# Optimization experiments

Hardware: AMD Instinct MI355X
Metric: run time of the kernel (lower is better)

The kernel has to match this reference:

```python
import jax, jax.numpy as jnp
import numpy as np

B, N_CITY, EC, VOCAB = 4096, 50, 128, 40000


def setup_inputs() -> dict:
    key = jax.random.key(0)
    k1, k2, k3, k4 = jax.random.split(key, 4)
    x = jax.random.normal(k1, (B, EC), dtype=jnp.float32)
    top_city_emb = jax.random.normal(k2, (B, N_CITY, EC), dtype=jnp.float32)
    top_city_id = jax.random.randint(k3, (B, N_CITY), 0, VOCAB)
    prob = jnp.zeros((B, VOCAB), dtype=jnp.float32)
    # nn.Linear(EC, EC) params
    W = jax.random.normal(k4, (EC, EC), dtype=jnp.float32) * (1.0 / np.sqrt(EC))
    b = jnp.zeros((EC,), dtype=jnp.float32)
    return {"x": x, "top_city_emb": top_city_emb, "top_city_id": top_city_id,
            "prob": prob, "W": W, "b": b}


def reference(x, top_city_emb, top_city_id, prob, W, b):
    # Linear projection (torch Linear: x @ W^T + b)
    emb_pred = x @ W.T + b                                  # [B, EC]
    # Broadcast dot-product score against candidate embeddings
    scores = jnp.einsum('be,bne->bn', emb_pred, top_city_emb)  # [B, N_CITY]
    p = jax.nn.softmax(scores, axis=1)                      # [B, N_CITY]
    # Scatter-add softmax probs into the vocab-sized output
    rows = jnp.arange(p.shape[0])[:, None]                  # [B, 1] -> broadcast to [B, N_CITY]
    rows = jnp.broadcast_to(rows, top_city_id.shape)
    out = jnp.zeros_like(prob).at[rows, top_city_id].add(p) + 1e-6
    return out
```

## Files before the change

### kernel.cpp

```cpp
#include <hip/hip_runtime.h>
#include <hip/hip_bf16.h>

#define NC    50
#define EC    128
#define VOCAB 40000

__global__ __launch_bounds__(256)
void EmbDotSoftMax_wtpack_kernel(const float* __restrict__ W,
                                 float4*      __restrict__ WTp)
{
    const int idx = blockIdx.x * 256 + threadIdx.x;
    if (idx < (EC / 4) * EC) {
        const int k4 = idx >> 7;
        const int e  = idx & 127;
        WTp[idx] = reinterpret_cast<const float4*>(W)[e * (EC / 4) + k4];
    }
}

__global__ __launch_bounds__(128)
void EmbDotSoftMax_scatter_kernel(const float*  __restrict__ x,
                                  const float*  __restrict__ emb,
                                  const int*    __restrict__ ids,
                                  const float4* __restrict__ WTp,
                                  const float*  __restrict__ bias,
                                  float*        __restrict__ out)
{
    const int b   = blockIdx.x;
    const int tid = threadIdx.x;
    const int w   = tid >> 6;
    const int l   = tid & 63;

    __shared__ float4 x_s4[EC / 4];
    __shared__ float  pred_s[EC];
    __shared__ float  score_s[NC];

    float* out_row = out + (size_t)b * VOCAB;

    if (tid < EC / 4)
        x_s4[tid] = reinterpret_cast<const float4*>(x + (size_t)b * EC)[tid];
    __syncthreads();

    const bool is_score_lane = (l < NC / 2);
    const int  city          = w * (NC / 2) + l;
    const float4* er =
        reinterpret_cast<const float4*>(emb + ((size_t)b * NC + city) * EC);
    float4 pf0, pf1, pf2, pf3, pf4, pf5, pf6, pf7;
    if (is_score_lane) {
        pf0 = er[0]; pf1 = er[1]; pf2 = er[2]; pf3 = er[3];
        pf4 = er[4]; pf5 = er[5]; pf6 = er[6]; pf7 = er[7];
    }

    {
        float acc = 0.0f;
        #pragma unroll
        for (int k4 = 0; k4 < EC / 4; ++k4) {
            const float4 wv = WTp[k4 * EC + tid];
            const float4 xv = x_s4[k4];
            acc = fmaf(wv.x, xv.x, acc);
            acc = fmaf(wv.y, xv.y, acc);
            acc = fmaf(wv.z, xv.z, acc);
            acc = fmaf(wv.w, xv.w, acc);
        }
        pred_s[tid] = acc + bias[tid];
    }
    __syncthreads();

    if (is_score_lane) {
        const float4* p4 = reinterpret_cast<const float4*>(pred_s);
        float acc = 0.0f;
        {
            float4 pv;
            pv = p4[0]; acc = fmaf(pf0.x, pv.x, acc); acc = fmaf(pf0.y, pv.y, acc);
                        acc = fmaf(pf0.z, pv.z, acc); acc = fmaf(pf0.w, pv.w, acc);
            pv = p4[1]; acc = fmaf(pf1.x, pv.x, acc); acc = fmaf(pf1.y, pv.y, acc);
                        acc = fmaf(pf1.z, pv.z, acc); acc = fmaf(pf1.w, pv.w, acc);
            pv = p4[2]; acc = fmaf(pf2.x, pv.x, acc); acc = fmaf(pf2.y, pv.y, acc);
                        acc = fmaf(pf2.z, pv.z, acc); acc = fmaf(pf2.w, pv.w, acc);
            pv = p4[3]; acc = fmaf(pf3.x, pv.x, acc); acc = fmaf(pf3.y, pv.y, acc);
                        acc = fmaf(pf3.z, pv.z, acc); acc = fmaf(pf3.w, pv.w, acc);
            pv = p4[4]; acc = fmaf(pf4.x, pv.x, acc); acc = fmaf(pf4.y, pv.y, acc);
                        acc = fmaf(pf4.z, pv.z, acc); acc = fmaf(pf4.w, pv.w, acc);
            pv = p4[5]; acc = fmaf(pf5.x, pv.x, acc); acc = fmaf(pf5.y, pv.y, acc);
                        acc = fmaf(pf5.z, pv.z, acc); acc = fmaf(pf5.w, pv.w, acc);
            pv = p4[6]; acc = fmaf(pf6.x, pv.x, acc); acc = fmaf(pf6.y, pv.y, acc);
                        acc = fmaf(pf6.z, pv.z, acc); acc = fmaf(pf6.w, pv.w, acc);
            pv = p4[7]; acc = fmaf(pf7.x, pv.x, acc); acc = fmaf(pf7.y, pv.y, acc);
                        acc = fmaf(pf7.z, pv.z, acc); acc = fmaf(pf7.w, pv.w, acc);
        }
        #pragma unroll
        for (int j = 8; j < EC / 4; ++j) {
            const float4 e4 = er[j];
            const float4 pv = p4[j];
            acc = fmaf(e4.x, pv.x, acc);
            acc = fmaf(e4.y, pv.y, acc);
            acc = fmaf(e4.z, pv.z, acc);
            acc = fmaf(e4.w, pv.w, acc);
        }
        score_s[city] = acc;
    }
    __syncthreads();

    if (tid < NC) {
        float m = -1e30f;
        #pragma unroll
        for (int n = 0; n < NC; ++n) m = fmaxf(m, score_s[n]);
        float sum = 0.0f;
        #pragma unroll
        for (int n = 0; n < NC; ++n) sum += __expf(score_s[n] - m);
        const float p  = __expf(score_s[tid] - m) / sum;
        const int   id = ids[(size_t)b * NC + tid];
        atomicAdd(out_row + id, p);
    }
}

__global__ __launch_bounds__(128)
void EmbDotSoftMax_scatter_fb(const float* __restrict__ x,
                              const float* __restrict__ emb,
                              const int*   __restrict__ ids,
                              const float* __restrict__ W,
                              const float* __restrict__ bias,
                              float*       __restrict__ out)
{
    const int b   = blockIdx.x;
    const int tid = threadIdx.x;
    const int w   = tid >> 6;
    const int l   = tid & 63;
    __shared__ float pred_s[EC];
    __shared__ float scores_s[NC];
    float* out_row = out + (size_t)b * VOCAB;
    {
        const float x0 = x[(size_t)b * EC + l];
        const float x1 = x[(size_t)b * EC + 64 + l];
        const float* Wbase = W + (size_t)w * 64 * EC;
        float mine = 0.0f;
        #pragma unroll 8
        for (int i = 0; i < 64; ++i) {
            const float* row = Wbase + i * EC;
            float part = fmaf(x0, row[l], x1 * row[l + 64]);
            #pragma unroll
            for (int off = 32; off; off >>= 1)
                part += __shfl_xor(part, off);
            if (i == l) mine = part;
        }
        pred_s[w * 64 + l] = mine + bias[w * 64 + l];
    }
    __syncthreads();
    {
        const float p0 = pred_s[l];
        const float p1 = pred_s[l + 64];
        const float* base = emb + (size_t)b * NC * EC + (size_t)w * (NC / 2) * EC;
        float part[NC / 2];
        #pragma unroll
        for (int i = 0; i < NC / 2; ++i) {
            const float* er2 = base + i * EC;
            part[i] = fmaf(p0, er2[l], p1 * er2[l + 64]);
        }
        #pragma unroll
        for (int off = 32; off; off >>= 1) {
            #pragma unroll
            for (int i = 0; i < NC / 2; ++i)
                part[i] += __shfl_xor(part[i], off);
        }
        if (l == 0) {
            #pragma unroll
            for (int i = 0; i < NC / 2; ++i)
                scores_s[w * (NC / 2) + i] = part[i];
        }
    }
    __syncthreads();
    if (tid < NC) {
        float m = -1e30f;
        #pragma unroll
        for (int n = 0; n < NC; ++n) m = fmaxf(m, scores_s[n]);
        float sum = 0.0f;
        #pragma unroll
        for (int n = 0; n < NC; ++n) sum += __expf(scores_s[n] - m);
        const float p = __expf(scores_s[tid] - m) / sum;
        atomicAdd(out_row + ids[(size_t)b * NC + tid], p);
    }
}

extern "C" void kernel_launch(void* const* d_in, const int* in_sizes, int n_in,
                              void* d_out, int out_size, void* d_ws, size_t ws_size,
                              hipStream_t stream) {
    const float* x    = (const float*)d_in[0];
    const float* emb  = (const float*)d_in[1];
    const int*   ids  = (const int*)d_in[2];
    const float* W    = (const float*)d_in[4];
    const float* bias = (const float*)d_in[5];
    float*       out  = (float*)d_out;

    const int B = in_sizes[0] / EC;
    const size_t ws_needed = (size_t)(EC / 4) * EC * sizeof(float4);

    hipMemsetAsync(d_out, 0, (size_t)out_size * sizeof(float), stream);

    if (ws_size >= ws_needed) {
        float4* WTp = (float4*)d_ws;
        hipLaunchKernelGGL(EmbDotSoftMax_wtpack_kernel,
                           dim3(16), dim3(256), 0, stream, W, WTp);
        hipLaunchKernelGGL(EmbDotSoftMax_scatter_kernel,
                           dim3(B), dim3(128), 0, stream,
                           x, emb, ids, WTp, bias, out);
    } else {
        hipLaunchKernelGGL(EmbDotSoftMax_scatter_fb,
                           dim3(B), dim3(128), 0, stream,
                           x, emb, ids, W, bias, out);
    }
}
```

Before: 167.7 us.

## Fuse output fill into compute kernel and defer scatter to merge pass

Replaces the separate memset with extra fill blocks inside a hybrid kernel. Those blocks write the 1e-6 baseline with float4 stores while other blocks run the projection, score and softmax for two rows each. The softmax probabilities go to a workspace buffer, and a small follow-up kernel scatter-adds them with atomics once the fill is done. The aim is to overlap the large output fill with the per-row compute and drop the memset launch. The cost is an extra kernel launch and a workspace round trip. The fill size is hardcoded and assumes B*VOCAB equals FILL_BLOCKS*256*40*4.

```diff
diff --git a/kernel.cpp b/kernel.cpp
--- a/kernel.cpp
+++ b/kernel.cpp
@@ -1,9 +1,10 @@
 #include <hip/hip_runtime.h>
 #include <hip/hip_bf16.h>
 
-#define NC    50
-#define EC    128
-#define VOCAB 40000
+#define NC          50
+#define EC          128
+#define VOCAB       40000
+#define FILL_BLOCKS 4000
 
 __global__ __launch_bounds__(256)
 void EmbDotSoftMax_wtpack_kernel(const float* __restrict__ W,
@@ -17,33 +18,45 @@
     }
 }
 
-__global__ __launch_bounds__(128)
-void EmbDotSoftMax_scatter_kernel(const float*  __restrict__ x,
-                                  const float*  __restrict__ emb,
-                                  const int*    __restrict__ ids,
-                                  const float4* __restrict__ WTp,
-                                  const float*  __restrict__ bias,
-                                  float*        __restrict__ out)
-{
-    const int b   = blockIdx.x;
+__global__ __launch_bounds__(256)
+void EmbDotSoftMax_hybrid_kernel(const float*  __restrict__ x,
+                                 const float*  __restrict__ emb,
+                                 const float4* __restrict__ WTp,
+                                 const float*  __restrict__ bias,
+                                 float*        __restrict__ out,
+                                 float*        __restrict__ pws)
+{
     const int tid = threadIdx.x;
-    const int w   = tid >> 6;
-    const int l   = tid & 63;
-
-    __shared__ float4 x_s4[EC / 4];
-    __shared__ float  pred_s[EC];
-    __shared__ float  score_s[NC];
-
-    float* out_row = out + (size_t)b * VOCAB;
-
-    if (tid < EC / 4)
-        x_s4[tid] = reinterpret_cast<const float4*>(x + (size_t)b * EC)[tid];
+
+    if (blockIdx.x < FILL_BLOCKS) {
+        const float4 fv = make_float4(1e-6f, 1e-6f, 1e-6f, 1e-6f);
+        float4* out4 = reinterpret_cast<float4*>(out);
+        const long stride = (long)FILL_BLOCKS * 256;
+        long idx = (long)blockIdx.x * 256 + tid;
+        #pragma unroll 4
+        for (int it = 0; it < 40; ++it, idx += stride)
+            out4[idx] = fv;
+        return;
+    }
+
+    const int half = tid >> 7;
+    const int t    = tid & 127;
+    const int r    = (blockIdx.x - FILL_BLOCKS) * 2 + half;
+    const int w    = t >> 6;
+    const int l    = t & 63;
+
+    __shared__ float4 x_s4[2][EC / 4];
+    __shared__ float  pred_s[2][EC];
+    __shared__ float  score_s[2][NC];
+
+    if (t < EC / 4)
+        x_s4[half][t] = reinterpret_cast<const float4*>(x + (size_t)r * EC)[t];
     __syncthreads();
 
     const bool is_score_lane = (l < NC / 2);
     const int  city          = w * (NC / 2) + l;
     const float4* er =
-        reinterpret_cast<const float4*>(emb + ((size_t)b * NC + city) * EC);
+        reinterpret_cast<const float4*>(emb + ((size_t)r * NC + city) * EC);
     float4 pf0, pf1, pf2, pf3, pf4, pf5, pf6, pf7;
     if (is_score_lane) {
         pf0 = er[0]; pf1 = er[1]; pf2 = er[2]; pf3 = er[3];
@@ -54,62 +67,72 @@
         float acc = 0.0f;
         #pragma unroll
         for (int k4 = 0; k4 < EC / 4; ++k4) {
-            const float4 wv = WTp[k4 * EC + tid];
-            const float4 xv = x_s4[k4];
+            const float4 wv = WTp[k4 * EC + t];
+            const float4 xv = x_s4[half][k4];
             acc = fmaf(wv.x, xv.x, acc);
             acc = fmaf(wv.y, xv.y, acc);
             acc = fmaf(wv.z, xv.z, acc);
             acc = fmaf(wv.w, xv.w, acc);
         }
-        pred_s[tid] = acc + bias[tid];
+        pred_s[half][t] = acc + bias[t];
     }
     __syncthreads();
 
     if (is_score_lane) {
-        const float4* p4 = reinterpret_cast<const float4*>(pred_s);
+        const float4* p4 = reinterpret_cast<const float4*>(pred_s[half]);
         float acc = 0.0f;
-        {
-            float4 pv;
-            pv = p4[0]; acc = fmaf(pf0.x, pv.x, acc); acc = fmaf(pf0.y, pv.y, acc);
-                        acc = fmaf(pf0.z, pv.z, acc); acc = fmaf(pf0.w, pv.w, acc);
-            pv = p4[1]; acc = fmaf(pf1.x, pv.x, acc); acc = fmaf(pf1.y, pv.y, acc);
-                        acc = fmaf(pf1.z, pv.z, acc); acc = fmaf(pf1.w, pv.w, acc);
-            pv = p4[2]; acc = fmaf(pf2.x, pv.x, acc); acc = fmaf(pf2.y, pv.y, acc);
-                        acc = fmaf(pf2.z, pv.z, acc); acc = fmaf(pf2.w, pv.w, acc);
-            pv = p4[3]; acc = fmaf(pf3.x, pv.x, acc); acc = fmaf(pf3.y, pv.y, acc);
-                        acc = fmaf(pf3.z, pv.z, acc); acc = fmaf(pf3.w, pv.w, acc);
-            pv = p4[4]; acc = fmaf(pf4.x, pv.x, acc); acc = fmaf(pf4.y, pv.y, acc);
-                        acc = fmaf(pf4.z, pv.z, acc); acc = fmaf(pf4.w, pv.w, acc);
-            pv = p4[5]; acc = fmaf(pf5.x, pv.x, acc); acc = fmaf(pf5.y, pv.y, acc);
-                        acc = fmaf(pf5.z, pv.z, acc); acc = fmaf(pf5.w, pv.w, acc);
-            pv = p4[6]; acc = fmaf(pf6.x, pv.x, acc); acc = fmaf(pf6.y, pv.y, acc);
-                        acc = fmaf(pf6.z, pv.z, acc); acc = fmaf(pf6.w, pv.w, acc);
-            pv = p4[7]; acc = fmaf(pf7.x, pv.x, acc); acc = fmaf(pf7.y, pv.y, acc);
-                        acc = fmaf(pf7.z, pv.z, acc); acc = fmaf(pf7.w, pv.w, acc);
-        }
+        float4 pv;
+        pv = p4[0]; acc = fmaf(pf0.x, pv.x, acc); acc = fmaf(pf0.y, pv.y, acc);
+                    acc = fmaf(pf0.z, pv.z, acc); acc = fmaf(pf0.w, pv.w, acc);
+        pv = p4[1]; acc = fmaf(pf1.x, pv.x, acc); acc = fmaf(pf1.y, pv.y, acc);
+                    acc = fmaf(pf1.z, pv.z, acc); acc = fmaf(pf1.w, pv.w, acc);
+        pv = p4[2]; acc = fmaf(pf2.x, pv.x, acc); acc = fmaf(pf2.y, pv.y, acc);
+                    acc = fmaf(pf2.z, pv.z, acc); acc = fmaf(pf2.w, pv.w, acc);
+        pv = p4[3]; acc = fmaf(pf3.x, pv.x, acc); acc = fmaf(pf3.y, pv.y, acc);
+                    acc = fmaf(pf3.z, pv.z, acc); acc = fmaf(pf3.w, pv.w, acc);
+        pv = p4[4]; acc = fmaf(pf4.x, pv.x, acc); acc = fmaf(pf4.y, pv.y, acc);
+                    acc = fmaf(pf4.z, pv.z, acc); acc = fmaf(pf4.w, pv.w, acc);
+        pv = p4[5]; acc = fmaf(pf5.x, pv.x, acc); acc = fmaf(pf5.y, pv.y, acc);
+                    acc = fmaf(pf5.z, pv.z, acc); acc = fmaf(pf5.w, pv.w, acc);
+        pv = p4[6]; acc = fmaf(pf6.x, pv.x, acc); acc = fmaf(pf6.y, pv.y, acc);
+                    acc = fmaf(pf6.z, pv.z, acc); acc = fmaf(pf6.w, pv.w, acc);
+        pv = p4[7]; acc = fmaf(pf7.x, pv.x, acc); acc = fmaf(pf7.y, pv.y, acc);
+                    acc = fmaf(pf7.z, pv.z, acc); acc = fmaf(pf7.w, pv.w, acc);
         #pragma unroll
         for (int j = 8; j < EC / 4; ++j) {
             const float4 e4 = er[j];
-            const float4 pv = p4[j];
-            acc = fmaf(e4.x, pv.x, acc);
-            acc = fmaf(e4.y, pv.y, acc);
-            acc = fmaf(e4.z, pv.z, acc);
-            acc = fmaf(e4.w, pv.w, acc);
-        }
-        score_s[city] = acc;
-    }
-    __syncthreads();
-
-    if (tid < NC) {
+            const float4 pp = p4[j];
+            acc = fmaf(e4.x, pp.x, acc);
+            acc = fmaf(e4.y, pp.y, acc);
+            acc = fmaf(e4.z, pp.z, acc);
+            acc = fmaf(e4.w, pp.w, acc);
+        }
+        score_s[half][city] = acc;
+    }
+    __syncthreads();
+
+    if (t < NC) {
         float m = -1e30f;
         #pragma unroll
-        for (int n = 0; n < NC; ++n) m = fmaxf(m, score_s[n]);
+        for (int n = 0; n < NC; ++n) m = fmaxf(m, score_s[half][n]);
         float sum = 0.0f;
         #pragma unroll
-        for (int n = 0; n < NC; ++n) sum += __expf(score_s[n] - m);
-        const float p  = __expf(score_s[tid] - m) / sum;
-        const int   id = ids[(size_t)b * NC + tid];
-        atomicAdd(out_row + id, p);
+        for (int n = 0; n < NC; ++n) sum += __expf(score_s[half][n] - m);
+        pws[(size_t)r * NC + t] = __expf(score_s[half][t] - m) / sum;
+    }
+}
+
+__global__ __launch_bounds__(256)
+void EmbDotSoftMax_merge_kernel(const int*   __restrict__ ids,
+                                const float* __restrict__ pws,
+                                float*       __restrict__ out,
+                                int total)
+{
+    const int t = blockIdx.x * 256 + threadIdx.x;
+    if (t < total) {
+        const int   b  = t / NC;
+        const int   id = ids[t];
+        atomicAdd(out + (size_t)b * VOCAB + id, pws[t]);
     }
 }
 
@@ -191,18 +214,22 @@
     float*       out  = (float*)d_out;
 
     const int B = in_sizes[0] / EC;
-    const size_t ws_needed = (size_t)(EC / 4) * EC * sizeof(float4);
-
-    hipMemsetAsync(d_out, 0, (size_t)out_size * sizeof(float), stream);
-
-    if (ws_size >= ws_needed) {
+    const size_t wtp_bytes = (size_t)(EC / 4) * EC * sizeof(float4);
+    const size_t pws_bytes = (size_t)B * NC * sizeof(float);
+
+    if (ws_size >= wtp_bytes + pws_bytes && (B % 2) == 0) {
         float4* WTp = (float4*)d_ws;
+        float*  pws = (float*)((char*)d_ws + wtp_bytes);
         hipLaunchKernelGGL(EmbDotSoftMax_wtpack_kernel,
                            dim3(16), dim3(256), 0, stream, W, WTp);
-        hipLaunchKernelGGL(EmbDotSoftMax_scatter_kernel,
-                           dim3(B), dim3(128), 0, stream,
-                           x, emb, ids, WTp, bias, out);
+        hipLaunchKernelGGL(EmbDotSoftMax_hybrid_kernel,
+                           dim3(FILL_BLOCKS + B / 2), dim3(256), 0, stream,
+                           x, emb, WTp, bias, out, pws);
+        hipLaunchKernelGGL(EmbDotSoftMax_merge_kernel,
+                           dim3((B * NC + 255) / 256), dim3(256), 0, stream,
+                           ids, pws, out, B * NC);
     } else {
+        hipMemsetAsync(d_out, 0, (size_t)out_size * sizeof(float), stream);
         hipLaunchKernelGGL(EmbDotSoftMax_scatter_fb,
                            dim3(B), dim3(128), 0, stream,
                            x, emb, ids, W, bias, out);
```

New measurement: 200.5 us. +19.5%, slower.
